# Performance work log

Hardware: AMD Instinct MI355X
Metric: run time of the kernel (lower is better)

The kernel has to match this reference:

```python
import jax, jax.numpy as jnp
import numpy as np

B, S, D, H, DFF = 4, 2048, 1024, 16, 4096
DK = D // H
EPS = 1e-6


def setup_inputs() -> dict:
    key = jax.random.key(0)
    ks = jax.random.split(key, 20)
    p = lambda k, shape: jax.random.normal(k, shape, dtype=jnp.float32) * 0.02
    inp = {
        "x": jax.random.normal(ks[0], (B, S, D), dtype=jnp.float32),
        "src_mask": jax.random.randint(ks[1], (B, 1, 1, S), 0, 2, dtype=jnp.int32),
        "Wq": p(ks[2], (D, D)), "bq": jnp.zeros((D,), jnp.float32),
        "Wk": p(ks[3], (D, D)), "bk": jnp.zeros((D,), jnp.float32),
        "Wv": p(ks[4], (D, D)), "bv": jnp.zeros((D,), jnp.float32),
        "Wo": p(ks[5], (D, D)), "bo": jnp.zeros((D,), jnp.float32),
        "W1": p(ks[6], (D, DFF)), "b1": jnp.zeros((DFF,), jnp.float32),
        "W2": p(ks[7], (DFF, D)), "b2": jnp.zeros((D,), jnp.float32),
        "ln1_a": jnp.ones((D,), jnp.float32), "ln1_b": jnp.zeros((D,), jnp.float32),
        "ln2_a": jnp.ones((D,), jnp.float32), "ln2_b": jnp.zeros((D,), jnp.float32),
    }
    return inp


def _layer_norm(x, a, b):
    # Faithful to source: unbiased std (torch default) and divide by (std + eps)
    mean = jnp.mean(x, axis=-1, keepdims=True)
    std = jnp.std(x, axis=-1, ddof=1, keepdims=True)
    return a * (x - mean) / (std + EPS) + b


def reference(x, src_mask, Wq, bq, Wk, bk, Wv, bv, Wo, bo, W1, b1, W2, b2,
              ln1_a, ln1_b, ln2_a, ln2_b):
    # Multi-head self-attention (dropout = identity, eval mode)
    q = (x @ Wq + bq).reshape(B, S, H, DK)
    k = (x @ Wk + bk).reshape(B, S, H, DK)
    v = (x @ Wv + bv).reshape(B, S, H, DK)
    scores = jnp.einsum("bqhd,bkhd->bhqk", q, k) / jnp.sqrt(jnp.float32(DK))
    scores = jnp.where(src_mask == 0, jnp.float32(-1e9), scores)
    attn = jax.nn.softmax(scores, axis=-1)
    ctx = jnp.einsum("bhqk,bkhd->bqhd", attn, v).reshape(B, S, D)
    attn_out = ctx @ Wo + bo

    x = _layer_norm(x + attn_out, ln1_a, ln1_b)

    # FeedForward: linear -> relu -> (dropout=identity) -> linear
    ff = jax.nn.relu(x @ W1 + b1) @ W2 + b2
    x = _layer_norm(x + ff, ln2_a, ln2_b)
    return x
```

## Files before the change

### kernel.cpp

```cpp
#include <hip/hip_runtime.h>

#define Bn 4
#define Sn 2048
#define Dn 1024
#define Hn 16
#define DKn 64
#define DFFn 4096
#define Mn (Bn * Sn)
#define QKVS 3072

typedef __bf16 bf16;
typedef __attribute__((ext_vector_type(8))) __bf16 bf16x8;
typedef __attribute__((ext_vector_type(4))) __bf16 bf16x4;
typedef __attribute__((ext_vector_type(8))) unsigned short u16x8;
typedef __attribute__((ext_vector_type(4))) float f32x4;
typedef __attribute__((ext_vector_type(16))) float f32x16;

#define LOG2E_DIV8 0.18033688011112042f

__device__ __forceinline__ float exp2fast(float x) {
  return __builtin_amdgcn_exp2f(x);
}

__device__ __forceinline__ void glds16(const bf16* g, bf16* l) {
  __builtin_amdgcn_global_load_lds((const __attribute__((address_space(1))) void*)g,
                                   (__attribute__((address_space(3))) void*)l, 16, 0, 0);
}

__device__ __forceinline__ unsigned int pkbf16(float a, float b) {
  union { __bf16 h[2]; unsigned int u; } x;
  x.h[0] = (__bf16)a; x.h[1] = (__bf16)b;
  return x.u;
}

__device__ __host__ __forceinline__ int bperm(int nl) {
  int wn = nl >> 6, rem = nl & 63, nf = rem >> 4, l = rem & 15;
  return ((nf >> 1) << 7) + (wn << 5) + ((nf & 1) << 4) + l;
}

__global__ __launch_bounds__(256) void k_cvt_bf16(const float* __restrict__ in,
                                                  bf16* __restrict__ out) {
  size_t i = ((size_t)blockIdx.x * 256 + threadIdx.x) * 8;
  f32x4 a = *(const f32x4*)(in + i);
  f32x4 b = *(const f32x4*)(in + i + 4);
  bf16x8 o;
#pragma unroll
  for (int j = 0; j < 4; ++j) { o[j] = (bf16)a[j]; o[j + 4] = (bf16)b[j]; }
  *(bf16x8*)(out + i) = o;
}

__global__ __launch_bounds__(256) void k_prep(const float* __restrict__ Wq,
                                              const float* __restrict__ Wk,
                                              const float* __restrict__ Wv,
                                              const float* __restrict__ Wo,
                                              const float* __restrict__ W1,
                                              const float* __restrict__ W2,
                                              const float* __restrict__ bq,
                                              const float* __restrict__ bk,
                                              const float* __restrict__ bv,
                                              bf16* __restrict__ wqkvT,
                                              bf16* __restrict__ woT,
                                              bf16* __restrict__ w1T,
                                              bf16* __restrict__ w2T,
                                              float* __restrict__ bqkv) {
  __shared__ float tile[32][33];
  const int id = blockIdx.x, t = threadIdx.x;
  if (id >= 12288) {
    int j = (id - 12288) * 256 + t;
    float v = (j < 1024) ? bq[j] * LOG2E_DIV8
            : (j < 2048) ? bk[j - 1024] : bv[j - 2048];
    bqkv[j] = v;
    return;
  }
  const float* in;
  bf16* out;
  int K, N, bx, by, perm;
  float scale = 1.f;
  if (id < 4096) {
    int z = id >> 10, local = id & 1023;
    bx = local & 31; by = local >> 5;
    K = Dn; N = Dn;
    if (z == 0)      { in = Wq; out = wqkvT; scale = LOG2E_DIV8; perm = 1; }
    else if (z == 1) { in = Wk; out = wqkvT + (size_t)1024 * Dn; perm = 1; }
    else if (z == 2) { in = Wv; out = wqkvT + (size_t)2048 * Dn; perm = 1; }
    else             { in = Wo; out = woT; perm = 0; }
  } else if (id < 8192) {
    int local = id - 4096;
    bx = local & 127; by = local >> 7;
    K = Dn; N = DFFn; in = W1; out = w1T; perm = 1;
  } else {
    int local = id - 8192;
    bx = local & 31; by = local >> 5;
    K = DFFn; N = Dn; in = W2; out = w2T; perm = 0;
  }
  const int n0 = bx * 32, k0 = by * 32;
  const int tx = t & 31, ty = t >> 5;
#pragma unroll
  for (int j = ty; j < 32; j += 8)
    tile[j][tx] = in[(size_t)(k0 + j) * N + n0 + tx];
  __syncthreads();
#pragma unroll
  for (int j = ty; j < 32; j += 8) {
    int row = n0 + j;
    if (perm) row = (row & ~255) | bperm(row & 255);
    out[(size_t)row * K + k0 + tx] = (bf16)(tile[tx][j] * scale);
  }
}

__global__ __launch_bounds__(256) void k_vt(const bf16* __restrict__ v,
                                            bf16* __restrict__ vT, int vs) {
  __shared__ bf16 T[64][72];
  const int t = threadIdx.x;
  const int s0 = blockIdx.x * 64;
  const int bh = blockIdx.y, b = bh >> 4, h = bh & 15;
#pragma unroll
  for (int it = 0; it < 2; ++it) {
    int r = (t >> 3) + it * 32;
    int c = t & 7;
    u16x8 val = *(const u16x8*)(v + (size_t)(b * Sn + s0 + r) * vs + h * 64 + c * 8);
    *(u16x8*)&T[r][c * 8] = val;
  }
  __syncthreads();
#pragma unroll
  for (int it = 0; it < 2; ++it) {
    int d = (t >> 3) + it * 32;
    int cs = t & 7;
    bf16x8 o;
#pragma unroll
    for (int j = 0; j < 8; ++j) o[j] = T[cs * 8 + j][d];
    *(bf16x8*)(vT + ((size_t)bh * 64 + d) * Sn + s0 + cs * 8) = o;
  }
}

template <int DO_RELU>
__global__ __launch_bounds__(512, 2) void k_gemm8ph(const bf16* __restrict__ A,
                                                    const bf16* __restrict__ BT,
                                                    const float* __restrict__ bias,
                                                    bf16* __restrict__ C,
                                                    int Ndim, int Kdim) {
  __shared__ __align__(128) bf16 Asm[2][256 * 64];
  __shared__ __align__(128) bf16 Bsm[2][256 * 64];
  const int tid = threadIdx.x;
  const int wid = tid >> 6, lane = tid & 63;
  const int l15 = lane & 15, l4 = lane >> 4;
  const int wm = wid >> 2, wn = wid & 3;

  const int gx = gridDim.x;
  int lin = blockIdx.y * gx + blockIdx.x;
  const int nwg = gx * gridDim.y;
  lin = (lin & 7) * (nwg >> 3) + (lin >> 3);
  const int m0 = (lin / gx) * 256;
  const int n0 = (lin % gx) * 256;

  f32x4 acc[8][4];
#pragma unroll
  for (int mf = 0; mf < 8; ++mf)
#pragma unroll
    for (int nf = 0; nf < 4; ++nf) acc[mf][nf] = f32x4{0.f, 0.f, 0.f, 0.f};

  const int lr = lane >> 3, lc = lane & 7;
  const int NT = Kdim >> 6;
  const int ch0 = lc ^ lr;

#define STGA(buf, t, it)                                                          \
  glds16(A + (size_t)(m0 + (it) * 64 + wid * 8 + lr) * Kdim + (size_t)(t) * 64 +  \
             ch0 * 8,                                                             \
         &Asm[buf][((it) * 64 + wid * 8) * 64]);
#define STGB(buf, t, it)                                                          \
  glds16(BT + (size_t)(n0 + (it) * 64 + wid * 8 + lr) * Kdim + (size_t)(t) * 64 + \
              ch0 * 8,                                                            \
         &Bsm[buf][((it) * 64 + wid * 8) * 64]);

  STGA(0, 0, 0); STGA(0, 0, 2);
  STGB(0, 0, 0); STGB(0, 0, 1);
  STGA(0, 0, 1); STGA(0, 0, 3);
  STGB(0, 0, 2); STGB(0, 0, 3);

  bf16x8 af[4][2], bl[2][2], bh2[2][2];

  for (int j = 0; j < NT; ++j) {
    const int d = j & 1, nb = d ^ 1;
    const bool st = (j + 1 < NT);

    asm volatile("s_waitcnt vmcnt(4)" ::: "memory");
    __builtin_amdgcn_sched_barrier(0);
    __builtin_amdgcn_s_barrier();
#pragma unroll
    for (int mf = 0; mf < 4; ++mf)
#pragma unroll
      for (int kk = 0; kk < 2; ++kk) {
        int row = wm * 128 + mf * 16 + l15;
        int ch = (kk * 4 + l4) ^ (row & 7);
        af[mf][kk] = *(const bf16x8*)&Asm[d][row * 64 + ch * 8];
      }
#pragma unroll
    for (int nf = 0; nf < 2; ++nf)
#pragma unroll
      for (int kk = 0; kk < 2; ++kk) {
        int row = wn * 32 + nf * 16 + l15;
        int ch = (kk * 4 + l4) ^ (row & 7);
        bl[nf][kk] = *(const bf16x8*)&Bsm[d][row * 64 + ch * 8];
      }
    if (st) { STGA(nb, j + 1, 0); STGA(nb, j + 1, 2); }
    __builtin_amdgcn_s_setprio(1);
#pragma unroll
    for (int mf = 0; mf < 4; ++mf)
#pragma unroll
      for (int nf = 0; nf < 2; ++nf)
#pragma unroll
        for (int kk = 0; kk < 2; ++kk)
          acc[mf][nf] = __builtin_amdgcn_mfma_f32_16x16x32_bf16(af[mf][kk], bl[nf][kk],
                                                                acc[mf][nf], 0, 0, 0);
    __builtin_amdgcn_s_setprio(0);

    if (st) asm volatile("s_waitcnt vmcnt(4)" ::: "memory");
    else    asm volatile("s_waitcnt vmcnt(2)" ::: "memory");
    __builtin_amdgcn_sched_barrier(0);
    __builtin_amdgcn_s_barrier();
#pragma unroll
    for (int mf = 0; mf < 4; ++mf)
#pragma unroll
      for (int kk = 0; kk < 2; ++kk) {
        int row = wm * 128 + 64 + mf * 16 + l15;
        int ch = (kk * 4 + l4) ^ (row & 7);
        af[mf][kk] = *(const bf16x8*)&Asm[d][row * 64 + ch * 8];
      }
    if (st) { STGB(nb, j + 1, 0); STGB(nb, j + 1, 1); }
    __builtin_amdgcn_s_setprio(1);
#pragma unroll
    for (int mf = 0; mf < 4; ++mf)
#pragma unroll
      for (int nf = 0; nf < 2; ++nf)
#pragma unroll
        for (int kk = 0; kk < 2; ++kk)
          acc[4 + mf][nf] = __builtin_amdgcn_mfma_f32_16x16x32_bf16(af[mf][kk], bl[nf][kk],
                                                                    acc[4 + mf][nf], 0, 0, 0);
    __builtin_amdgcn_s_setprio(0);

    if (st) asm volatile("s_waitcnt vmcnt(4)" ::: "memory");
    else    asm volatile("s_waitcnt vmcnt(0)" ::: "memory");
    __builtin_amdgcn_sched_barrier(0);
    __builtin_amdgcn_s_barrier();
#pragma unroll
    for (int nf = 0; nf < 2; ++nf)
#pragma unroll
      for (int kk = 0; kk < 2; ++kk) {
        int row = 128 + wn * 32 + nf * 16 + l15;
        int ch = (kk * 4 + l4) ^ (row & 7);
        bh2[nf][kk] = *(const bf16x8*)&Bsm[d][row * 64 + ch * 8];
      }
    if (st) { STGA(nb, j + 1, 1); STGA(nb, j + 1, 3); }
    __builtin_amdgcn_s_setprio(1);
#pragma unroll
    for (int mf = 0; mf < 4; ++mf)
#pragma unroll
      for (int nf = 0; nf < 2; ++nf)
#pragma unroll
        for (int kk = 0; kk < 2; ++kk)
          acc[4 + mf][2 + nf] = __builtin_amdgcn_mfma_f32_16x16x32_bf16(
              af[mf][kk], bh2[nf][kk], acc[4 + mf][2 + nf], 0, 0, 0);
    __builtin_amdgcn_s_setprio(0);

#pragma unroll
    for (int mf = 0; mf < 4; ++mf)
#pragma unroll
      for (int kk = 0; kk < 2; ++kk) {
        int row = wm * 128 + mf * 16 + l15;
        int ch = (kk * 4 + l4) ^ (row & 7);
        af[mf][kk] = *(const bf16x8*)&Asm[d][row * 64 + ch * 8];
      }
    if (st) { STGB(nb, j + 1, 2); STGB(nb, j + 1, 3); }
    __builtin_amdgcn_s_setprio(1);
#pragma unroll
    for (int mf = 0; mf < 4; ++mf)
#pragma unroll
      for (int nf = 0; nf < 2; ++nf)
#pragma unroll
        for (int kk = 0; kk < 2; ++kk)
          acc[mf][2 + nf] = __builtin_amdgcn_mfma_f32_16x16x32_bf16(
              af[mf][kk], bh2[nf][kk], acc[mf][2 + nf], 0, 0, 0);
    __builtin_amdgcn_s_setprio(0);
  }
#undef STGA
#undef STGB

#pragma unroll
  for (int mf = 0; mf < 8; ++mf)
#pragma unroll
    for (int nf = 0; nf < 4; ++nf) {
      int c = n0 + wn * 64 + nf * 16 + l15;
      float bv = bias[c];
      int r0 = m0 + wm * 128 + mf * 16 + l4 * 4;
#pragma unroll
      for (int r = 0; r < 4; ++r) {
        float val = acc[mf][nf][r] + bv;
        if (DO_RELU) val = fmaxf(val, 0.f);
        C[(size_t)(r0 + r) * Ndim + c] = (bf16)val;
      }
    }
}

template <int NFRAG, int DO_RELU>
__global__ __launch_bounds__(512, 2) void k_gemm256(const bf16* __restrict__ A,
                                                    const bf16* __restrict__ BT,
                                                    const float* __restrict__ bias,
                                                    bf16* __restrict__ C,
                                                    int Ndim, int Kdim) {
  __shared__ __align__(128) bf16 Asm[2][256 * 64];
  __shared__ __align__(128) bf16 Bsm[2][NFRAG * 64 * 64];
  const int tid = threadIdx.x;
  const int wid = tid >> 6, lane = tid & 63;
  const int l15 = lane & 15, l4 = lane >> 4;
  const int wm = wid >> 2, wn = wid & 3;

  const int gx = gridDim.x;
  int lin = blockIdx.y * gx + blockIdx.x;
  const int nwg = gx * gridDim.y;
  lin = (lin & 7) * (nwg >> 3) + (lin >> 3);
  const int m0 = (lin / gx) * 256;
  const int n0 = (lin % gx) * (NFRAG * 64);

  f32x4 acc[8][NFRAG];
#pragma unroll
  for (int mf = 0; mf < 8; ++mf)
#pragma unroll
    for (int nf = 0; nf < NFRAG; ++nf) acc[mf][nf] = f32x4{0.f, 0.f, 0.f, 0.f};

  const int lr = lane >> 3, lc = lane & 7;
  const int NT = Kdim >> 6;

#define STAGE(buf, t)                                                              \
  {                                                                                \
    _Pragma("unroll") for (int it = 0; it < 4; ++it) {                             \
      int r = it * 64 + wid * 8 + lr;                                              \
      int ch = lc ^ (r & 7);                                                       \
      glds16(A + (size_t)(m0 + r) * Kdim + (size_t)(t) * 64 + ch * 8,              \
             &Asm[buf][(it * 64 + wid * 8) * 64]);                                 \
    }                                                                              \
    _Pragma("unroll") for (int it = 0; it < NFRAG; ++it) {                         \
      int r = it * 64 + wid * 8 + lr;                                              \
      int ch = lc ^ (r & 7);                                                       \
      glds16(BT + (size_t)(n0 + r) * Kdim + (size_t)(t) * 64 + ch * 8,             \
             &Bsm[buf][(it * 64 + wid * 8) * 64]);                                 \
    }                                                                              \
  }

  int p = 0;
  STAGE(0, 0);
  for (int t = 0; t < NT; ++t) {
    if (t + 1 < NT) {
      STAGE(p ^ 1, t + 1);
      if constexpr (NFRAG == 4) asm volatile("s_waitcnt vmcnt(8)" ::: "memory");
      else                      asm volatile("s_waitcnt vmcnt(6)" ::: "memory");
    } else {
      asm volatile("s_waitcnt vmcnt(0)" ::: "memory");
    }
    __builtin_amdgcn_sched_barrier(0);
    __builtin_amdgcn_s_barrier();

    bf16x8 bfrag[NFRAG][2];
#pragma unroll
    for (int nf = 0; nf < NFRAG; ++nf)
#pragma unroll
      for (int kk = 0; kk < 2; ++kk) {
        int r = wn * (NFRAG * 16) + nf * 16 + l15;
        int ch = (kk * 4 + l4) ^ (r & 7);
        bfrag[nf][kk] = *(const bf16x8*)&Bsm[p][r * 64 + ch * 8];
      }
#pragma unroll
    for (int half = 0; half < 2; ++half) {
      bf16x8 afr[4][2];
#pragma unroll
      for (int mf4 = 0; mf4 < 4; ++mf4)
#pragma unroll
        for (int kk = 0; kk < 2; ++kk) {
          int r = wm * 128 + half * 64 + mf4 * 16 + l15;
          int ch = (kk * 4 + l4) ^ (r & 7);
          afr[mf4][kk] = *(const bf16x8*)&Asm[p][r * 64 + ch * 8];
        }
      __builtin_amdgcn_s_setprio(1);
#pragma unroll
      for (int mf4 = 0; mf4 < 4; ++mf4)
#pragma unroll
        for (int nf = 0; nf < NFRAG; ++nf)
#pragma unroll
          for (int kk = 0; kk < 2; ++kk)
            acc[half * 4 + mf4][nf] = __builtin_amdgcn_mfma_f32_16x16x32_bf16(
                afr[mf4][kk], bfrag[nf][kk], acc[half * 4 + mf4][nf], 0, 0, 0);
      __builtin_amdgcn_s_setprio(0);
    }
    __builtin_amdgcn_s_barrier();
    p ^= 1;
  }
#undef STAGE

#pragma unroll
  for (int mf = 0; mf < 8; ++mf)
#pragma unroll
    for (int nf = 0; nf < NFRAG; ++nf) {
      int c = n0 + wn * (NFRAG * 16) + nf * 16 + l15;
      float bv = bias[c];
      int r0 = m0 + wm * 128 + mf * 16 + l4 * 4;
#pragma unroll
      for (int r = 0; r < 4; ++r) {
        float val = acc[mf][nf][r] + bv;
        if (DO_RELU) val = fmaxf(val, 0.f);
        C[(size_t)(r0 + r) * Ndim + c] = (bf16)val;
      }
    }
}

__global__ __launch_bounds__(512) void k_attn(const bf16* __restrict__ q,
                                              const bf16* __restrict__ k,
                                              const bf16* __restrict__ vT,
                                              const int* __restrict__ mask,
                                              bf16* __restrict__ ctx, int qs) {
  __shared__ __align__(128) bf16 Kt[2][64 * 64];
  __shared__ __align__(128) bf16 Vt[2][64 * 64];
  __shared__ float Mb[Sn];
  const int tid = threadIdx.x, wid = tid >> 6, lane = tid & 63;
  const int q31 = lane & 31, hi = lane >> 5;

  int lin = blockIdx.y * gridDim.x + blockIdx.x;
  lin = (lin & 7) * 64 + (lin >> 3);
  const int qblk = lin & 7, bh = lin >> 3;
  const int b = bh >> 4, h = bh & 15;
  const int q0 = qblk * 256 + wid * 32;

  for (int i = tid; i < Sn; i += 512)
    Mb[i] = mask[b * Sn + i] ? 0.f : -1.44269504e9f;

  bf16x8 qf[4];
#pragma unroll
  for (int t = 0; t < 4; ++t)
    qf[t] = *(const bf16x8*)(q + (size_t)(b * Sn + q0 + q31) * qs + h * 64 +
                             t * 16 + hi * 8);

  f32x16 o[2];
  o[0] = {}; o[1] = {};
  float mr = -INFINITY, lr = 0.f;

  const int lrow = lane >> 3;
  const int lch0 = lane & 7;
  const int sch = lch0 ^ (lrow ^ (wid & 3));

  for (int kb = 0; kb < Sn / 64; ++kb) {
    const int cur = kb & 1;
    if (kb == 0) {
      int row = wid * 8 + lrow;
      glds16(k + (size_t)(b * Sn + row) * qs + h * 64 + sch * 8, &Kt[0][wid * 512]);
      glds16(vT + ((size_t)bh * 64 + row) * Sn + sch * 8, &Vt[0][wid * 512]);
      __syncthreads();
    }
    if (kb + 1 < Sn / 64) {
      int row = wid * 8 + lrow;
      glds16(k + (size_t)(b * Sn + (kb + 1) * 64 + row) * qs + h * 64 + sch * 8,
             &Kt[cur ^ 1][wid * 512]);
      glds16(vT + ((size_t)bh * 64 + row) * Sn + (kb + 1) * 64 + sch * 8,
             &Vt[cur ^ 1][wid * 512]);
    }

    f32x16 sc[2];
#pragma unroll
    for (int kf = 0; kf < 2; ++kf)
#pragma unroll
      for (int rg = 0; rg < 4; ++rg) {
        f32x4 mb4 = *(const f32x4*)&Mb[kb * 64 + kf * 32 + rg * 8 + 4 * hi];
#pragma unroll
        for (int j = 0; j < 4; ++j) sc[kf][rg * 4 + j] = mb4[j];
      }
#pragma unroll
    for (int t = 0; t < 4; ++t) {
#pragma unroll
      for (int kf = 0; kf < 2; ++kf) {
        int row = kf * 32 + q31;
        int ch = (t * 2 + hi) ^ ((row & 7) ^ ((row >> 3) & 3));
        bf16x8 kfr = *(const bf16x8*)&Kt[cur][row * 64 + ch * 8];
        sc[kf] = __builtin_amdgcn_mfma_f32_32x32x16_bf16(kfr, qf[t], sc[kf], 0, 0, 0);
      }
    }

    float rmax = fmaxf(sc[0][0], sc[0][1]);
#pragma unroll
    for (int i = 2; i < 16; i += 2)
      rmax = fmaxf(fmaxf(rmax, sc[0][i]), sc[0][i + 1]);
#pragma unroll
    for (int i = 0; i < 16; i += 2)
      rmax = fmaxf(fmaxf(rmax, sc[1][i]), sc[1][i + 1]);
    rmax = fmaxf(rmax, __shfl_xor(rmax, 32));

    if (!__all(rmax <= mr + 8.f)) {
      float mnew = fmaxf(mr, rmax);
      float psc = exp2fast(mr - mnew);
      mr = mnew;
      lr *= psc;
#pragma unroll
      for (int af = 0; af < 2; ++af)
#pragma unroll
        for (int i = 0; i < 16; ++i) o[af][i] *= psc;
    }

    float psum = 0.f;
#pragma unroll
    for (int kf = 0; kf < 2; ++kf)
#pragma unroll
      for (int i = 0; i < 16; ++i) {
        float p = exp2fast(sc[kf][i] - mr);
        sc[kf][i] = p;
        psum += p;
      }
    psum += __shfl_xor(psum, 32);
    lr += psum;

#pragma unroll
    for (int ks = 0; ks < 4; ++ks) {
      const int kf = ks >> 1, R = (ks & 1) * 8;
      unsigned int a0 = pkbf16(sc[kf][R + 0], sc[kf][R + 1]);
      unsigned int a1 = pkbf16(sc[kf][R + 2], sc[kf][R + 3]);
      unsigned int b0 = pkbf16(sc[kf][R + 4], sc[kf][R + 5]);
      unsigned int b1 = pkbf16(sc[kf][R + 6], sc[kf][R + 7]);
      asm volatile("v_permlane32_swap_b32 %0, %1" : "+v"(a0), "+v"(b0));
      asm volatile("v_permlane32_swap_b32 %0, %1" : "+v"(a1), "+v"(b1));
      union { unsigned int w[4]; bf16x8 v; } pfu;
      pfu.w[0] = a0;
      pfu.w[1] = a1;
      pfu.w[2] = b0;
      pfu.w[3] = b1;
#pragma unroll
      for (int af = 0; af < 2; ++af) {
        int row = af * 32 + q31;
        int ch = (ks * 2 + hi) ^ ((row & 7) ^ ((row >> 3) & 3));
        bf16x8 vfr = *(const bf16x8*)&Vt[cur][row * 64 + ch * 8];
        o[af] = __builtin_amdgcn_mfma_f32_32x32x16_bf16(vfr, pfu.v, o[af], 0, 0, 0);
      }
    }
    __syncthreads();
  }

  float inv = 1.f / lr;
  const size_t cbase = (size_t)(b * Sn + q0 + q31) * Dn + h * 64;
#pragma unroll
  for (int af = 0; af < 2; ++af)
#pragma unroll
    for (int rg = 0; rg < 4; ++rg) {
      bf16x4 ov;
#pragma unroll
      for (int j = 0; j < 4; ++j) ov[j] = (bf16)(o[af][rg * 4 + j] * inv);
      *(bf16x4*)(ctx + cbase + af * 32 + rg * 8 + 4 * hi) = ov;
    }
}

template <int XF32, int OUTF32>
__global__ __launch_bounds__(256) void k_ln(const void* __restrict__ xp,
                                            const bf16* __restrict__ res,
                                            const float* __restrict__ gamma,
                                            const float* __restrict__ beta,
                                            void* __restrict__ yout) {
  const int row = blockIdx.x, t = threadIdx.x;
  const size_t base = (size_t)row * Dn + t * 4;
  f32x4 a;
  if constexpr (XF32) {
    a = *(const f32x4*)((const float*)xp + base);
  } else {
    bf16x4 x4 = *(const bf16x4*)((const bf16*)xp + base);
#pragma unroll
    for (int j = 0; j < 4; ++j) a[j] = (float)x4[j];
  }
  bf16x4 rb = *(const bf16x4*)(res + base);
  f32x4 vv;
#pragma unroll
  for (int j = 0; j < 4; ++j) vv[j] = a[j] + (float)rb[j];

  float s = vv[0] + vv[1] + vv[2] + vv[3];
#pragma unroll
  for (int off = 32; off; off >>= 1) s += __shfl_xor(s, off);
  __shared__ float red1[4], red2[4];
  if ((t & 63) == 0) red1[t >> 6] = s;
  __syncthreads();
  float mean = (red1[0] + red1[1] + red1[2] + red1[3]) * (1.f / 1024.f);

  float d[4], s2 = 0.f;
#pragma unroll
  for (int j = 0; j < 4; ++j) { d[j] = vv[j] - mean; s2 += d[j] * d[j]; }
#pragma unroll
  for (int off = 32; off; off >>= 1) s2 += __shfl_xor(s2, off);
  if ((t & 63) == 0) red2[t >> 6] = s2;
  __syncthreads();
  float var = (red2[0] + red2[1] + red2[2] + red2[3]) * (1.f / 1023.f);
  float inv = 1.f / (sqrtf(var) + 1e-6f);

  f32x4 g = *(const f32x4*)(gamma + t * 4);
  f32x4 bt = *(const f32x4*)(beta + t * 4);
#pragma unroll
  for (int j = 0; j < 4; ++j) d[j] = g[j] * d[j] * inv + bt[j];
  if constexpr (OUTF32) {
    f32x4 outv = {d[0], d[1], d[2], d[3]};
    *(f32x4*)((float*)yout + base) = outv;
  } else {
    bf16x4 outb;
#pragma unroll
    for (int j = 0; j < 4; ++j) outb[j] = (bf16)d[j];
    *(bf16x4*)((bf16*)yout + base) = outb;
  }
}

extern "C" void kernel_launch(void* const* d_in, const int* in_sizes, int n_in,
                              void* d_out, int out_size, void* d_ws, size_t ws_size,
                              hipStream_t stream) {
  const float* x   = (const float*)d_in[0];
  const int*   msk = (const int*)d_in[1];
  const float* Wq  = (const float*)d_in[2];
  const float* bq  = (const float*)d_in[3];
  const float* Wk  = (const float*)d_in[4];
  const float* bk  = (const float*)d_in[5];
  const float* Wv  = (const float*)d_in[6];
  const float* bv  = (const float*)d_in[7];
  const float* Wo  = (const float*)d_in[8];
  const float* bo  = (const float*)d_in[9];
  const float* W1  = (const float*)d_in[10];
  const float* b1  = (const float*)d_in[11];
  const float* W2  = (const float*)d_in[12];
  const float* b2  = (const float*)d_in[13];
  const float* g1  = (const float*)d_in[14];
  const float* be1 = (const float*)d_in[15];
  const float* g2  = (const float*)d_in[16];
  const float* be2 = (const float*)d_in[17];
  float* out = (float*)d_out;

  char* w = (char*)d_ws;
  size_t off = 0;
  auto alloc = [&](size_t bytes) { void* p = w + off; off += (bytes + 255) & ~(size_t)255; return p; };
  bf16* xb    = (bf16*)alloc((size_t)Mn * Dn * 2);
  bf16* wqkvT = (bf16*)alloc((size_t)QKVS * Dn * 2);
  bf16* woT   = (bf16*)alloc((size_t)Dn * Dn * 2);
  bf16* w1T   = (bf16*)alloc((size_t)Dn * DFFn * 2);
  bf16* w2T   = (bf16*)alloc((size_t)DFFn * Dn * 2);
  float* bqkv = (float*)alloc((size_t)QKVS * 4);
  bf16* qkv   = (bf16*)alloc((size_t)Mn * QKVS * 2);
  bf16* ctx   = (bf16*)alloc((size_t)Mn * Dn * 2);
  bf16* attnb = (bf16*)alloc((size_t)Mn * Dn * 2);
  bf16* yb    = (bf16*)alloc((size_t)Mn * Dn * 2);
  (void)ws_size; (void)in_sizes; (void)n_in; (void)out_size;
  bf16* vT = xb;
  bf16* hh = qkv;
  bf16* ff = xb;

  k_cvt_bf16<<<(Mn * Dn) / 2048, 256, 0, stream>>>(x, xb);
  k_prep<<<12300, 256, 0, stream>>>(Wq, Wk, Wv, Wo, W1, W2, bq, bk, bv,
                                    wqkvT, woT, w1T, w2T, bqkv);

  k_gemm8ph<0><<<dim3(QKVS / 256, Mn / 256), 512, 0, stream>>>(xb, wqkvT, bqkv, qkv, QKVS, Dn);

  k_vt<<<dim3(Sn / 64, Bn * Hn), 256, 0, stream>>>(qkv + 2048, vT, QKVS);
  k_attn<<<dim3(Sn / 256, Bn * Hn), 512, 0, stream>>>(qkv, qkv + 1024, vT, msk, ctx, QKVS);

  k_gemm256<2, 0><<<dim3(Dn / 128, Mn / 256), 512, 0, stream>>>(ctx, woT, bo, attnb, Dn, Dn);

  k_ln<1, 0><<<Mn, 256, 0, stream>>>(x, attnb, g1, be1, yb);

  k_gemm8ph<1><<<dim3(DFFn / 256, Mn / 256), 512, 0, stream>>>(yb, w1T, b1, hh, DFFn, Dn);

  k_gemm256<2, 0><<<dim3(Dn / 128, Mn / 256), 512, 0, stream>>>(hh, w2T, b2, ff, Dn, DFFn);

  k_ln<0, 1><<<Mn, 256, 0, stream>>>(yb, ff, g2, be2, out);
}
```

Baseline: 391.0 us.

## Use four-phase interleaved pipeline for 256x128 output-projection and FFN2 GEMMs

Replaces the double-buffered k_gemm256<2> with a new k_gemm8ph128 kernel. Each K step is split into four phases that interleave LDS fragment reads, partial global-to-LDS staging of the next tile, and MFMA quadrants, each phase guarded by its own waitcnt and barrier. The Wo and W2 weights are pre-permuted with a new bperm128 row mapping so each wave's B rows sit contiguously in the new layout. The aim is to overlap memory staging with compute more finely, at the cost of more barriers per K step and tighter vmcnt bookkeeping.

```diff
diff --git a/kernel.cpp b/kernel.cpp
--- a/kernel.cpp
+++ b/kernel.cpp
@@ -36,6 +36,10 @@
 __device__ __host__ __forceinline__ int bperm(int nl) {
   int wn = nl >> 6, rem = nl & 63, nf = rem >> 4, l = rem & 15;
   return ((nf >> 1) << 7) + (wn << 5) + ((nf & 1) << 4) + l;
+}
+__device__ __host__ __forceinline__ int bperm128(int nl) {
+  int wn = nl >> 5, nf = (nl >> 4) & 1, l = nl & 15;
+  return (nf << 6) + (wn << 4) + l;
 }
 
 __global__ __launch_bounds__(256) void k_cvt_bf16(const float* __restrict__ in,
@@ -83,7 +87,7 @@
     if (z == 0)      { in = Wq; out = wqkvT; scale = LOG2E_DIV8; perm = 1; }
     else if (z == 1) { in = Wk; out = wqkvT + (size_t)1024 * Dn; perm = 1; }
     else if (z == 2) { in = Wv; out = wqkvT + (size_t)2048 * Dn; perm = 1; }
-    else             { in = Wo; out = woT; perm = 0; }
+    else             { in = Wo; out = woT; perm = 2; }
   } else if (id < 8192) {
     int local = id - 4096;
     bx = local & 127; by = local >> 7;
@@ -91,7 +95,7 @@
   } else {
     int local = id - 8192;
     bx = local & 31; by = local >> 5;
-    K = DFFn; N = Dn; in = W2; out = w2T; perm = 0;
+    K = DFFn; N = Dn; in = W2; out = w2T; perm = 2;
   }
   const int n0 = bx * 32, k0 = by * 32;
   const int tx = t & 31, ty = t >> 5;
@@ -102,7 +106,8 @@
 #pragma unroll
   for (int j = ty; j < 32; j += 8) {
     int row = n0 + j;
-    if (perm) row = (row & ~255) | bperm(row & 255);
+    if (perm == 1) row = (row & ~255) | bperm(row & 255);
+    else if (perm == 2) row = (row & ~127) | bperm128(row & 127);
     out[(size_t)row * K + k0 + tx] = (bf16)(tile[tx][j] * scale);
   }
 }
@@ -300,14 +305,14 @@
     }
 }
 
-template <int NFRAG, int DO_RELU>
-__global__ __launch_bounds__(512, 2) void k_gemm256(const bf16* __restrict__ A,
-                                                    const bf16* __restrict__ BT,
-                                                    const float* __restrict__ bias,
-                                                    bf16* __restrict__ C,
-                                                    int Ndim, int Kdim) {
+template <int DO_RELU>
+__global__ __launch_bounds__(512, 2) void k_gemm8ph128(const bf16* __restrict__ A,
+                                                       const bf16* __restrict__ BT,
+                                                       const float* __restrict__ bias,
+                                                       bf16* __restrict__ C,
+                                                       int Ndim, int Kdim) {
   __shared__ __align__(128) bf16 Asm[2][256 * 64];
-  __shared__ __align__(128) bf16 Bsm[2][NFRAG * 64 * 64];
+  __shared__ __align__(128) bf16 Bsm[2][128 * 64];
   const int tid = threadIdx.x;
   const int wid = tid >> 6, lane = tid & 63;
   const int l15 = lane & 15, l4 = lane >> 4;
@@ -318,87 +323,133 @@
   const int nwg = gx * gridDim.y;
   lin = (lin & 7) * (nwg >> 3) + (lin >> 3);
   const int m0 = (lin / gx) * 256;
-  const int n0 = (lin % gx) * (NFRAG * 64);
-
-  f32x4 acc[8][NFRAG];
+  const int n0 = (lin % gx) * 128;
+
+  f32x4 acc[8][2];
 #pragma unroll
   for (int mf = 0; mf < 8; ++mf)
 #pragma unroll
-    for (int nf = 0; nf < NFRAG; ++nf) acc[mf][nf] = f32x4{0.f, 0.f, 0.f, 0.f};
+    for (int nf = 0; nf < 2; ++nf) acc[mf][nf] = f32x4{0.f, 0.f, 0.f, 0.f};
 
   const int lr = lane >> 3, lc = lane & 7;
   const int NT = Kdim >> 6;
-
-#define STAGE(buf, t)                                                              \
-  {                                                                                \
-    _Pragma("unroll") for (int it = 0; it < 4; ++it) {                             \
-      int r = it * 64 + wid * 8 + lr;                                              \
-      int ch = lc ^ (r & 7);                                                       \
-      glds16(A + (size_t)(m0 + r) * Kdim + (size_t)(t) * 64 + ch * 8,              \
-             &Asm[buf][(it * 64 + wid * 8) * 64]);                                 \
-    }                                                                              \
-    _Pragma("unroll") for (int it = 0; it < NFRAG; ++it) {                         \
-      int r = it * 64 + wid * 8 + lr;                                              \
-      int ch = lc ^ (r & 7);                                                       \
-      glds16(BT + (size_t)(n0 + r) * Kdim + (size_t)(t) * 64 + ch * 8,             \
-             &Bsm[buf][(it * 64 + wid * 8) * 64]);                                 \
-    }                                                                              \
-  }
-
-  int p = 0;
-  STAGE(0, 0);
-  for (int t = 0; t < NT; ++t) {
-    if (t + 1 < NT) {
-      STAGE(p ^ 1, t + 1);
-      if constexpr (NFRAG == 4) asm volatile("s_waitcnt vmcnt(8)" ::: "memory");
-      else                      asm volatile("s_waitcnt vmcnt(6)" ::: "memory");
-    } else {
-      asm volatile("s_waitcnt vmcnt(0)" ::: "memory");
-    }
+  const int ch0 = lc ^ lr;
+
+#define STGA(buf, t, it)                                                          \
+  glds16(A + (size_t)(m0 + (it) * 64 + wid * 8 + lr) * Kdim + (size_t)(t) * 64 +  \
+             ch0 * 8,                                                             \
+         &Asm[buf][((it) * 64 + wid * 8) * 64]);
+#define STGB(buf, t, it)                                                          \
+  glds16(BT + (size_t)(n0 + (it) * 64 + wid * 8 + lr) * Kdim + (size_t)(t) * 64 + \
+              ch0 * 8,                                                            \
+         &Bsm[buf][((it) * 64 + wid * 8) * 64]);
+
+  STGA(0, 0, 0); STGA(0, 0, 2);
+  STGB(0, 0, 0);
+  STGA(0, 0, 1); STGA(0, 0, 3);
+  STGB(0, 0, 1);
+
+  bf16x8 af[4][2], bl[2], bh2[2];
+
+  for (int j = 0; j < NT; ++j) {
+    const int d = j & 1, nb = d ^ 1;
+    const bool st = (j + 1 < NT);
+
+    asm volatile("s_waitcnt vmcnt(3)" ::: "memory");
     __builtin_amdgcn_sched_barrier(0);
     __builtin_amdgcn_s_barrier();
-
-    bf16x8 bfrag[NFRAG][2];
-#pragma unroll
-    for (int nf = 0; nf < NFRAG; ++nf)
+#pragma unroll
+    for (int mf = 0; mf < 4; ++mf)
 #pragma unroll
       for (int kk = 0; kk < 2; ++kk) {
-        int r = wn * (NFRAG * 16) + nf * 16 + l15;
-        int ch = (kk * 4 + l4) ^ (r & 7);
-        bfrag[nf][kk] = *(const bf16x8*)&Bsm[p][r * 64 + ch * 8];
-      }
-#pragma unroll
-    for (int half = 0; half < 2; ++half) {
-      bf16x8 afr[4][2];
-#pragma unroll
-      for (int mf4 = 0; mf4 < 4; ++mf4)
-#pragma unroll
-        for (int kk = 0; kk < 2; ++kk) {
-          int r = wm * 128 + half * 64 + mf4 * 16 + l15;
-          int ch = (kk * 4 + l4) ^ (r & 7);
-          afr[mf4][kk] = *(const bf16x8*)&Asm[p][r * 64 + ch * 8];
-        }
-      __builtin_amdgcn_s_setprio(1);
-#pragma unroll
-      for (int mf4 = 0; mf4 < 4; ++mf4)
-#pragma unroll
-        for (int nf = 0; nf < NFRAG; ++nf)
-#pragma unroll
-          for (int kk = 0; kk < 2; ++kk)
-            acc[half * 4 + mf4][nf] = __builtin_amdgcn_mfma_f32_16x16x32_bf16(
-                afr[mf4][kk], bfrag[nf][kk], acc[half * 4 + mf4][nf], 0, 0, 0);
-      __builtin_amdgcn_s_setprio(0);
-    }
+        int row = wm * 128 + mf * 16 + l15;
+        int ch = (kk * 4 + l4) ^ (row & 7);
+        af[mf][kk] = *(const bf16x8*)&Asm[d][row * 64 + ch * 8];
+      }
+#pragma unroll
+    for (int kk = 0; kk < 2; ++kk) {
+      int row = wn * 16 + l15;
+      int ch = (kk * 4 + l4) ^ (row & 7);
+      bl[kk] = *(const bf16x8*)&Bsm[d][row * 64 + ch * 8];
+    }
+    if (st) { STGA(nb, j + 1, 0); STGA(nb, j + 1, 2); }
+    __builtin_amdgcn_s_setprio(1);
+#pragma unroll
+    for (int mf = 0; mf < 4; ++mf)
+#pragma unroll
+      for (int kk = 0; kk < 2; ++kk)
+        acc[mf][0] = __builtin_amdgcn_mfma_f32_16x16x32_bf16(af[mf][kk], bl[kk],
+                                                             acc[mf][0], 0, 0, 0);
+    __builtin_amdgcn_s_setprio(0);
+
+    if (st) asm volatile("s_waitcnt vmcnt(3)" ::: "memory");
+    else    asm volatile("s_waitcnt vmcnt(1)" ::: "memory");
+    __builtin_amdgcn_sched_barrier(0);
     __builtin_amdgcn_s_barrier();
-    p ^= 1;
-  }
-#undef STAGE
+#pragma unroll
+    for (int mf = 0; mf < 4; ++mf)
+#pragma unroll
+      for (int kk = 0; kk < 2; ++kk) {
+        int row = wm * 128 + 64 + mf * 16 + l15;
+        int ch = (kk * 4 + l4) ^ (row & 7);
+        af[mf][kk] = *(const bf16x8*)&Asm[d][row * 64 + ch * 8];
+      }
+    if (st) STGB(nb, j + 1, 0);
+    __builtin_amdgcn_s_setprio(1);
+#pragma unroll
+    for (int mf = 0; mf < 4; ++mf)
+#pragma unroll
+      for (int kk = 0; kk < 2; ++kk)
+        acc[4 + mf][0] = __builtin_amdgcn_mfma_f32_16x16x32_bf16(af[mf][kk], bl[kk],
+                                                                 acc[4 + mf][0], 0, 0, 0);
+    __builtin_amdgcn_s_setprio(0);
+
+    if (st) asm volatile("s_waitcnt vmcnt(3)" ::: "memory");
+    else    asm volatile("s_waitcnt vmcnt(0)" ::: "memory");
+    __builtin_amdgcn_sched_barrier(0);
+    __builtin_amdgcn_s_barrier();
+#pragma unroll
+    for (int kk = 0; kk < 2; ++kk) {
+      int row = 64 + wn * 16 + l15;
+      int ch = (kk * 4 + l4) ^ (row & 7);
+      bh2[kk] = *(const bf16x8*)&Bsm[d][row * 64 + ch * 8];
+    }
+    if (st) { STGA(nb, j + 1, 1); STGA(nb, j + 1, 3); }
+    __builtin_amdgcn_s_setprio(1);
+#pragma unroll
+    for (int mf = 0; mf < 4; ++mf)
+#pragma unroll
+      for (int kk = 0; kk < 2; ++kk)
+        acc[4 + mf][1] = __builtin_amdgcn_mfma_f32_16x16x32_bf16(af[mf][kk], bh2[kk],
+                                                                 acc[4 + mf][1], 0, 0, 0);
+    __builtin_amdgcn_s_setprio(0);
+
+#pragma unroll
+    for (int mf = 0; mf < 4; ++mf)
+#pragma unroll
+      for (int kk = 0; kk < 2; ++kk) {
+        int row = wm * 128 + mf * 16 + l15;
+        int ch = (kk * 4 + l4) ^ (row & 7);
+        af[mf][kk] = *(const bf16x8*)&Asm[d][row * 64 + ch * 8];
+      }
+    if (st) STGB(nb, j + 1, 1);
+    __builtin_amdgcn_s_setprio(1);
+#pragma unroll
+    for (int mf = 0; mf < 4; ++mf)
+#pragma unroll
+      for (int kk = 0; kk < 2; ++kk)
+        acc[mf][1] = __builtin_amdgcn_mfma_f32_16x16x32_bf16(af[mf][kk], bh2[kk],
+                                                             acc[mf][1], 0, 0, 0);
+    __builtin_amdgcn_s_setprio(0);
+  }
+#undef STGA
+#undef STGB
 
 #pragma unroll
   for (int mf = 0; mf < 8; ++mf)
 #pragma unroll
-    for (int nf = 0; nf < NFRAG; ++nf) {
-      int c = n0 + wn * (NFRAG * 16) + nf * 16 + l15;
+    for (int nf = 0; nf < 2; ++nf) {
+      int c = n0 + wn * 32 + nf * 16 + l15;
       float bv = bias[c];
       int r0 = m0 + wm * 128 + mf * 16 + l4 * 4;
 #pragma unroll
@@ -654,13 +705,13 @@
   k_vt<<<dim3(Sn / 64, Bn * Hn), 256, 0, stream>>>(qkv + 2048, vT, QKVS);
   k_attn<<<dim3(Sn / 256, Bn * Hn), 512, 0, stream>>>(qkv, qkv + 1024, vT, msk, ctx, QKVS);
 
-  k_gemm256<2, 0><<<dim3(Dn / 128, Mn / 256), 512, 0, stream>>>(ctx, woT, bo, attnb, Dn, Dn);
+  k_gemm8ph128<0><<<dim3(Dn / 128, Mn / 256), 512, 0, stream>>>(ctx, woT, bo, attnb, Dn, Dn);
 
   k_ln<1, 0><<<Mn, 256, 0, stream>>>(x, attnb, g1, be1, yb);
 
   k_gemm8ph<1><<<dim3(DFFn / 256, Mn / 256), 512, 0, stream>>>(yb, w1T, b1, hh, DFFn, Dn);
 
-  k_gemm256<2, 0><<<dim3(Dn / 128, Mn / 256), 512, 0, stream>>>(hh, w2T, b2, ff, Dn, DFFn);
+  k_gemm8ph128<0><<<dim3(Dn / 128, Mn / 256), 512, 0, stream>>>(hh, w2T, b2, ff, Dn, DFFn);
 
   k_ln<0, 1><<<Mn, 256, 0, stream>>>(yb, ff, g2, be2, out);
 }
```

Result: slower. 400.3 us (+2.4%).
